# Optimization experiments

Hardware: AMD Instinct MI355X
Metric: run time of the kernel (lower is better)

The kernel has to match this reference:

```python
import jax, jax.numpy as jnp
import numpy as np

SIGMA = 1
KSIZE = SIGMA * 4 + 1  # 5
EPS = 1e-5

def _gauss_kernel1d(ksize, sigma):
    half = (ksize - 1) * 0.5
    x = jnp.linspace(-half, half, ksize)
    pdf = jnp.exp(-0.5 * (x / sigma) ** 2)
    return pdf / pdf.sum()

def _blur_axis(x, kernel, axis):
    # 'same' zero-padded 1D correlation along `axis` (grouped conv equivalent)
    pad = (kernel.shape[0] - 1) // 2
    cfg = [(0, 0)] * x.ndim
    cfg[axis] = (pad, pad)
    xp = jnp.pad(x, cfg)
    n = x.shape[axis]
    out = jnp.zeros_like(x)
    for i in range(kernel.shape[0]):
        out = out + kernel[i] * jax.lax.slice_in_dim(xp, i, i + n, axis=axis)
    return out

def gaussian_blur3d(x):  # x: [B,C,D,H,W]
    k = _gauss_kernel1d(KSIZE, SIGMA).astype(x.dtype)
    for ax in (2, 3, 4):
        x = _blur_axis(x, k, ax)
    return x

def lncc(I, J):
    bI, bJ = gaussian_blur3d(I), gaussian_blur3d(J)
    cross = gaussian_blur3d(I * J) - bI * bJ
    varI = jax.nn.relu(gaussian_blur3d(I * I) - bI ** 2) + EPS
    varJ = jax.nn.relu(gaussian_blur3d(J * J) - bJ ** 2) + EPS
    return jnp.mean(1.0 - cross / jnp.sqrt(varI * varJ))

def warp(img, phi):
    # trilinear grid_sample, zeros padding, align_corners=True
    # img: [B,C,D,H,W]; phi: [B,3,D,H,W] normalized coords (z,y,x) in [-1,1]
    B, C, D, H, W = img.shape
    scale = jnp.array([D - 1, H - 1, W - 1], img.dtype).reshape(1, 3, 1, 1, 1)
    coords = (phi + 1.0) * 0.5 * scale
    z, y, x = coords[:, 0], coords[:, 1], coords[:, 2]
    z0 = jnp.floor(z).astype(jnp.int32)
    y0 = jnp.floor(y).astype(jnp.int32)
    x0 = jnp.floor(x).astype(jnp.int32)
    fz, fy, fx = z - z0, y - y0, x - x0
    gather = jax.vmap(lambda im, zz, yy, xx: im[:, zz, yy, xx])
    out = jnp.zeros((B, C, D, H, W), img.dtype)
    for dz in (0, 1):
        for dy in (0, 1):
            for dx in (0, 1):
                zi, yi, xi = z0 + dz, y0 + dy, x0 + dx
                w = (fz if dz else 1 - fz) * (fy if dy else 1 - fy) * (fx if dx else 1 - fx)
                valid = ((zi >= 0) & (zi < D) & (yi >= 0) & (yi < H) & (xi >= 0) & (xi < W)).astype(img.dtype)
                zc = jnp.clip(zi, 0, D - 1)
                yc = jnp.clip(yi, 0, H - 1)
                xc = jnp.clip(xi, 0, W - 1)
                out = out + gather(img, zc, yc, xc) * (w * valid)[:, None]
    return out

def dice_loss(a, b):
    B = a.shape[0]
    af = a.reshape(B, -1)
    bf = b.reshape(B, -1)
    inter = jnp.sum(af * bf, axis=1)
    dice = (2.0 * inter + EPS) / (jnp.sum(af, axis=1) + jnp.sum(bf, axis=1) + EPS)
    return jnp.mean(1.0 - dice)

def identity_grid(size, batch, dtype):
    axes = [jnp.linspace(-1.0, 1.0, s, dtype=dtype) for s in size]
    grid = jnp.stack(jnp.meshgrid(*axes, indexing='ij'), axis=0)  # [3,D,H,W]
    return jnp.broadcast_to(grid[None], (batch,) + grid.shape)

def mse(a, b):
    return jnp.mean((a - b) ** 2)

def setup_inputs() -> dict:
    key = jax.random.key(0)
    ks = jax.random.split(key, 7)
    D = 128
    sp = (1, 3, D, D, D)
    si = (1, 1, D, D, D)
    return {
        'phi_AB': jax.random.normal(ks[0], sp, jnp.float32),
        'phi_BA': jax.random.normal(ks[1], sp, jnp.float32),
        'image_A': jax.random.normal(ks[2], si, jnp.float32),
        'image_B': jax.random.normal(ks[3], si, jnp.float32),
        'label_A': jax.random.uniform(ks[4], si, jnp.float32),
        'label_B': jax.random.uniform(ks[5], si, jnp.float32),
        'noise': jax.random.normal(ks[6], sp, jnp.float32),
    }

def reference(phi_AB, phi_BA, image_A, image_B, label_A, label_B, noise):
    lam = 128.0
    B = phi_AB.shape[0]
    size = phi_AB.shape[2:]
    idg = identity_grid(size, B, phi_AB.dtype)
    Ieps = idg + noise * (1.0 / size[-1])
    fwd = warp(warp(Ieps, phi_AB), phi_BA)
    bwd = warp(warp(Ieps, phi_BA), phi_AB)
    ic_loss = mse(Ieps, fwd) + mse(Ieps, bwd)
    warped_A = warp(image_A, phi_AB)
    warped_B = warp(image_B, phi_BA)
    sim_loss = lncc(warped_A, image_B) + lncc(image_A, warped_B)
    wlA = warp(label_A, phi_AB)
    wlB = warp(label_B, phi_BA)
    d_loss = dice_loss(wlA, label_B) + dice_loss(label_A, wlB)
    return lam * ic_loss + sim_loss + d_loss
```

## Files before the change

kernel.cpp:

```cpp
#include <hip/hip_runtime.h>


#define DSZ 128
#define DD  (DSZ*DSZ)
#define NVOX (DSZ*DSZ*DSZ)
#define NBLK (NVOX/256)
#define EPSF 1e-5f

#define KW0 0.054488684549642945f
#define KW1 0.24420134200323337f
#define KW2 0.40261994689424736f
#define KW3 0.24420134200323337f
#define KW4 0.054488684549642945f

#define PSTRIDE 8192

__device__ __forceinline__ double warp_red(double v) {
#pragma unroll
  for (int o = 32; o > 0; o >>= 1) v += __shfl_down(v, o, 64);
  return v;
}

__device__ __forceinline__ void block_part1(double a, double* p) {
  __shared__ double s[4];
  const int lane = threadIdx.x & 63, wid = threadIdx.x >> 6;
  a = warp_red(a);
  if (lane == 0) s[wid] = a;
  __syncthreads();
  if (threadIdx.x == 0) p[blockIdx.x] = s[0] + s[1] + s[2] + s[3];
}

__device__ __forceinline__ void block_part3(double a, double b, double c,
                                            double* p0, double* p1, double* p2) {
  __shared__ double s[3][4];
  const int lane = threadIdx.x & 63, wid = threadIdx.x >> 6;
  a = warp_red(a); b = warp_red(b); c = warp_red(c);
  if (lane == 0) { s[0][wid] = a; s[1][wid] = b; s[2][wid] = c; }
  __syncthreads();
  if (threadIdx.x == 0) {
    p0[blockIdx.x] = s[0][0] + s[0][1] + s[0][2] + s[0][3];
    p1[blockIdx.x] = s[1][0] + s[1][1] + s[1][2] + s[1][3];
    p2[blockIdx.x] = s[2][0] + s[2][1] + s[2][2] + s[2][3];
  }
}

__global__ void __launch_bounds__(256) k_pack(
    const float* __restrict__ noise, const float* __restrict__ imgA,
    const float* __restrict__ labA, const float* __restrict__ imgB,
    const float* __restrict__ labB, float4* __restrict__ S) {
  const int v = blockIdx.x * 256 + threadIdx.x;
  float4 a, b;
  a.x = noise[v]; a.y = noise[NVOX + v]; a.z = noise[2*NVOX + v]; a.w = imgA[v];
  b.x = labA[v];  b.y = imgB[v];         b.z = labB[v];           b.w = 0.0f;
  S[2*v] = a; S[2*v + 1] = b;
}

struct AxisPrep {
  int c0, c1;
  float w0, w1;
};
__device__ __forceinline__ AxisPrep axis_prep(float p) {
  AxisPrep r;
  const float pf = floorf(p);
  const int i0 = (int)pf;
  const float f = p - pf;
  const bool v0 = (i0 >= 0) && (i0 < DSZ);
  const bool v1 = (i0 + 1 >= 0) && (i0 + 1 < DSZ);
  r.c0 = min(max(i0, 0), DSZ - 1);
  r.c1 = min(max(i0 + 1, 0), DSZ - 1);
  r.w0 = v0 ? (1.0f - f) : 0.0f;
  r.w1 = v1 ? f : 0.0f;
  return r;
}

__global__ void __launch_bounds__(256) k_warp_first(
    const float* __restrict__ phiAB, const float* __restrict__ phiBA,
    const float4* __restrict__ S,
    const float* __restrict__ labA, const float* __restrict__ labB,
    float4* __restrict__ W1, float4* __restrict__ W2,
    float* __restrict__ wA, float* __restrict__ wB,
    double* __restrict__ P) {
  const int dir = blockIdx.y;
  const float* __restrict__ phi  = dir ? phiBA : phiAB;
  const float* __restrict__ olbl = dir ? labA  : labB;
  float4* __restrict__ W    = dir ? W2 : W1;
  float*  __restrict__ wimg = dir ? wB : wA;
  double* __restrict__ p    = P + (size_t)(dir ? 3 : 0) * PSTRIDE;

  const int v = blockIdx.x * 256 + threadIdx.x;
  const float ob = olbl[v];
  const float z = (phi[v]          + 1.0f) * 0.5f * 127.0f;
  const float y = (phi[NVOX + v]   + 1.0f) * 0.5f * 127.0f;
  const float x = (phi[2*NVOX + v] + 1.0f) * 0.5f * 127.0f;
  const int z0 = (int)floorf(z), y0 = (int)floorf(y), x0 = (int)floorf(x);
  float o0 = 0.f, o1 = 0.f, o2 = 0.f, oi = 0.f, ol = 0.f;
  if (z0 >= -1 && z0 < DSZ && y0 >= -1 && y0 < DSZ && x0 >= -1 && x0 < DSZ) {
    const AxisPrep az = axis_prep(z), ay = axis_prep(y), ax = axis_prep(x);
    const int zc[2] = {az.c0, az.c1}; const float wz[2] = {az.w0, az.w1};
    const int yc[2] = {ay.c0, ay.c1}; const float wy[2] = {ay.w0, ay.w1};
    const int xc[2] = {ax.c0, ax.c1}; const float wx[2] = {ax.w0, ax.w1};

    float4 g0[8], g1[8];
#pragma unroll
    for (int k = 0; k < 8; k++) {
      const int idx = zc[k >> 2] * DD + yc[(k >> 1) & 1] * DSZ + xc[k & 1];
      g0[k] = S[2 * idx];
      g1[k] = S[2 * idx + 1];
    }
#pragma unroll
    for (int k = 0; k < 8; k++) {
      const int iz = zc[k >> 2], iy = yc[(k >> 1) & 1], ix = xc[k & 1];
      const float w = wz[k >> 2] * wy[(k >> 1) & 1] * wx[k & 1];
      const float e0 = (-1.0f + iz * (2.0f/127.0f)) + g0[k].x * (1.0f/128.0f);
      const float e1 = (-1.0f + iy * (2.0f/127.0f)) + g0[k].y * (1.0f/128.0f);
      const float e2 = (-1.0f + ix * (2.0f/127.0f)) + g0[k].z * (1.0f/128.0f);
      o0 += e0 * w; o1 += e1 * w; o2 += e2 * w;
      const float iv = dir ? g1[k].y : g0[k].w;
      const float lv = dir ? g1[k].z : g1[k].x;
      oi += iv * w;
      ol += lv * w;
    }
  }
  W[v] = make_float4(o0, o1, o2, 0.0f);
  wimg[v] = oi;
  block_part3((double)(ol * ob), (double)ol, (double)ob,
              p, p + PSTRIDE, p + 2 * PSTRIDE);
}

__global__ void __launch_bounds__(256) k_warp_second_mse(
    const float* __restrict__ phiAB, const float* __restrict__ phiBA,
    const float4* __restrict__ W1, const float4* __restrict__ W2,
    const float* __restrict__ noise, double* __restrict__ P) {
  const int dir = blockIdx.y;
  const float* __restrict__ phi   = dir ? phiAB : phiBA;
  const float4* __restrict__ Wsrc = dir ? W2 : W1;
  double* __restrict__ p = P + (size_t)(6 + dir) * PSTRIDE;

  const int v = blockIdx.x * 256 + threadIdx.x;
  const float z = (phi[v]          + 1.0f) * 0.5f * 127.0f;
  const float y = (phi[NVOX + v]   + 1.0f) * 0.5f * 127.0f;
  const float x = (phi[2*NVOX + v] + 1.0f) * 0.5f * 127.0f;
  const int z0 = (int)floorf(z), y0 = (int)floorf(y), x0 = (int)floorf(x);
  float f0 = 0.f, f1 = 0.f, f2 = 0.f;
  if (z0 >= -1 && z0 < DSZ && y0 >= -1 && y0 < DSZ && x0 >= -1 && x0 < DSZ) {
    const AxisPrep az = axis_prep(z), ay = axis_prep(y), ax = axis_prep(x);
    const int zc[2] = {az.c0, az.c1}; const float wz[2] = {az.w0, az.w1};
    const int yc[2] = {ay.c0, ay.c1}; const float wy[2] = {ay.w0, ay.w1};
    const int xc[2] = {ax.c0, ax.c1}; const float wx[2] = {ax.w0, ax.w1};

    float4 g[8];
#pragma unroll
    for (int k = 0; k < 8; k++) {
      const int idx = zc[k >> 2] * DD + yc[(k >> 1) & 1] * DSZ + xc[k & 1];
      g[k] = Wsrc[idx];
    }
#pragma unroll
    for (int k = 0; k < 8; k++) {
      const float w = wz[k >> 2] * wy[(k >> 1) & 1] * wx[k & 1];
      f0 += g[k].x * w; f1 += g[k].y * w; f2 += g[k].z * w;
    }
  }
  const int zi = v >> 14, yi = (v >> 7) & 127, xi = v & 127;
  const float e0 = (-1.0f + zi * (2.0f/127.0f)) + noise[v]          * (1.0f/128.0f);
  const float e1 = (-1.0f + yi * (2.0f/127.0f)) + noise[NVOX + v]   * (1.0f/128.0f);
  const float e2 = (-1.0f + xi * (2.0f/127.0f)) + noise[2*NVOX + v] * (1.0f/128.0f);
  const float d0 = e0 - f0, d1 = e1 - f1, d2 = e2 - f2;
  block_part1((double)(d0*d0) + (double)(d1*d1) + (double)(d2*d2), p);
}

__global__ void __launch_bounds__(256) k_lncc(
    const float* __restrict__ wA, const float* __restrict__ imgB,
    const float* __restrict__ imgA, const float* __restrict__ wB,
    double* __restrict__ P) {
  const int pair = blockIdx.y;
  const float* __restrict__ I = pair ? imgA : wA;
  const float* __restrict__ J = pair ? wB : imgB;
  double* __restrict__ p = P + (size_t)(8 + pair) * PSTRIDE;

  const int bx = blockIdx.x;
  const int zi = bx & 127;
  const int y0 = (bx >> 7) * 8;

  __shared__ float zb[5][12][128];
  __shared__ float yb[5][8][128];
  const int t = threadIdx.x;
  const float K[5] = {KW0, KW1, KW2, KW3, KW4};

  for (int pp = t; pp < 12 * 128; pp += 256) {
    const int r = pp >> 7, x = pp & 127;
    const int y = y0 + r - 2;
    float a0 = 0.f, a1 = 0.f, a2 = 0.f, a3 = 0.f, a4 = 0.f;
    if (y >= 0 && y < DSZ) {
      const int base = y * DSZ + x;
#pragma unroll
      for (int s = 0; s < 5; s++) {
        const int zz = zi + s - 2;
        if (zz >= 0 && zz < DSZ) {
          const float iv = I[zz * DD + base], jv = J[zz * DD + base];
          const float k = K[s];
          a0 += k * iv; a1 += k * jv; a2 += k * (iv * jv);
          a3 += k * (iv * iv); a4 += k * (jv * jv);
        }
      }
    }
    zb[0][r][x] = a0; zb[1][r][x] = a1; zb[2][r][x] = a2;
    zb[3][r][x] = a3; zb[4][r][x] = a4;
  }
  __syncthreads();

  for (int pp = t; pp < 8 * 128; pp += 256) {
    const int r = pp >> 7, x = pp & 127;
#pragma unroll
    for (int c = 0; c < 5; c++) {
      yb[c][r][x] = KW0 * zb[c][r][x] + KW1 * zb[c][r + 1][x] + KW2 * zb[c][r + 2][x]
                  + KW3 * zb[c][r + 3][x] + KW4 * zb[c][r + 4][x];
    }
  }
  __syncthreads();

  double lsum = 0.0;
  for (int pp = t; pp < 8 * 128; pp += 256) {
    const int r = pp >> 7, x = pp & 127;
    float b[5];
#pragma unroll
    for (int c = 0; c < 5; c++) {
      float s = 0.f;
#pragma unroll
      for (int u = 0; u < 5; u++) {
        const int xx = x + u - 2;
        if (xx >= 0 && xx < DSZ) s += K[u] * yb[c][r][xx];
      }
      b[c] = s;
    }
    const float cross = b[2] - b[0] * b[1];
    const float varI = fmaxf(b[3] - b[0] * b[0], 0.0f) + EPSF;
    const float varJ = fmaxf(b[4] - b[1] * b[1], 0.0f) + EPSF;
    lsum += (double)(1.0f - cross / sqrtf(varI * varJ));
  }
  block_part1(lsum, p);
}

__global__ void __launch_bounds__(256) k_reduce(
    const double* __restrict__ P, double* __restrict__ acc) {
  const int c = blockIdx.x;
  const int n = (c >= 8) ? 2048 : 8192;
  const double* src = P + (size_t)c * PSTRIDE;
  double s = 0.0;
  for (int i = threadIdx.x; i < n; i += 256) s += src[i];
  __shared__ double sh[4];
  const int lane = threadIdx.x & 63, wid = threadIdx.x >> 6;
  s = warp_red(s);
  if (lane == 0) sh[wid] = s;
  __syncthreads();
  if (threadIdx.x == 0) acc[c] = sh[0] + sh[1] + sh[2] + sh[3];
}

__global__ void k_final(const double* __restrict__ acc, float* __restrict__ out) {
  const double n1 = (double)NVOX;
  const double n3 = 3.0 * n1;
  const double ic  = acc[6] / n3 + acc[7] / n3;
  const double sim = acc[8] / n1 + acc[9] / n1;
  const double dA = (2.0 * acc[0] + 1e-5) / (acc[1] + acc[2] + 1e-5);
  const double dB = (2.0 * acc[3] + 1e-5) / (acc[4] + acc[5] + 1e-5);
  out[0] = (float)(128.0 * ic + sim + (1.0 - dA) + (1.0 - dB));
}

extern "C" void kernel_launch(void* const* d_in, const int* in_sizes, int n_in,
                              void* d_out, int out_size, void* d_ws, size_t ws_size,
                              hipStream_t stream) {
  (void)in_sizes; (void)n_in; (void)out_size; (void)ws_size;
  const float* phiAB = (const float*)d_in[0];
  const float* phiBA = (const float*)d_in[1];
  const float* imgA  = (const float*)d_in[2];
  const float* imgB  = (const float*)d_in[3];
  const float* labA  = (const float*)d_in[4];
  const float* labB  = (const float*)d_in[5];
  const float* noise = (const float*)d_in[6];
  float* out = (float*)d_out;

  char* ws = (char*)d_ws;
  double* acc = (double*)ws;
  double* P   = acc + 16;
  float4* S  = (float4*)(ws + (1 << 20));
  float4* W1 = S + 2 * (size_t)NVOX;
  float4* W2 = W1 + (size_t)NVOX;
  float*  wA = (float*)(W2 + (size_t)NVOX);
  float*  wB = wA + NVOX;

  k_pack<<<NBLK, 256, 0, stream>>>(noise, imgA, labA, imgB, labB, S);

  k_warp_first<<<dim3(NBLK, 2), 256, 0, stream>>>(
      phiAB, phiBA, S, labA, labB, W1, W2, wA, wB, P);

  k_warp_second_mse<<<dim3(NBLK, 2), 256, 0, stream>>>(
      phiAB, phiBA, W1, W2, noise, P);

  k_lncc<<<dim3(2048, 2), 256, 0, stream>>>(wA, imgB, imgA, wB, P);

  k_reduce<<<10, 256, 0, stream>>>(P, acc);

  k_final<<<1, 1, 0, stream>>>(acc, out);
}
```

Before: 487.3 us.

## Fuse second warp/MSE and LNCC into one interleaved kernel launch

Merges the second-warp MSE kernel and the LNCC blur kernel into one launch. Blocks are interleaved two warp blocks to one LNCC block, so the gather-bound and compute/LDS-bound work can share the GPU at the same time. The LNCC tile is halved from 8 to 4 rows per block, which doubles its block count and raises the z/y halo overhead. Shared-memory allocation is now the union of both paths, which may reduce occupancy for the warp blocks.

```diff
diff --git a/kernel.cpp b/kernel.cpp
--- a/kernel.cpp
+++ b/kernel.cpp
@@ -21,26 +21,27 @@
   return v;
 }
 
-__device__ __forceinline__ void block_part1(double a, double* p) {
-  __shared__ double s[4];
+__device__ __forceinline__ void block_part1(double a, double* p, int slot) {
+  __shared__ double s1[4];
   const int lane = threadIdx.x & 63, wid = threadIdx.x >> 6;
   a = warp_red(a);
-  if (lane == 0) s[wid] = a;
+  if (lane == 0) s1[wid] = a;
   __syncthreads();
-  if (threadIdx.x == 0) p[blockIdx.x] = s[0] + s[1] + s[2] + s[3];
+  if (threadIdx.x == 0) p[slot] = s1[0] + s1[1] + s1[2] + s1[3];
 }
 
 __device__ __forceinline__ void block_part3(double a, double b, double c,
-                                            double* p0, double* p1, double* p2) {
-  __shared__ double s[3][4];
+                                            double* p0, double* p1, double* p2,
+                                            int slot) {
+  __shared__ double s3[3][4];
   const int lane = threadIdx.x & 63, wid = threadIdx.x >> 6;
   a = warp_red(a); b = warp_red(b); c = warp_red(c);
-  if (lane == 0) { s[0][wid] = a; s[1][wid] = b; s[2][wid] = c; }
+  if (lane == 0) { s3[0][wid] = a; s3[1][wid] = b; s3[2][wid] = c; }
   __syncthreads();
   if (threadIdx.x == 0) {
-    p0[blockIdx.x] = s[0][0] + s[0][1] + s[0][2] + s[0][3];
-    p1[blockIdx.x] = s[1][0] + s[1][1] + s[1][2] + s[1][3];
-    p2[blockIdx.x] = s[2][0] + s[2][1] + s[2][2] + s[2][3];
+    p0[slot] = s3[0][0] + s3[0][1] + s3[0][2] + s3[0][3];
+    p1[slot] = s3[1][0] + s3[1][1] + s3[1][2] + s3[1][3];
+    p2[slot] = s3[2][0] + s3[2][1] + s3[2][2] + s3[2][3];
   }
 }
 
@@ -124,126 +125,131 @@
   W[v] = make_float4(o0, o1, o2, 0.0f);
   wimg[v] = oi;
   block_part3((double)(ol * ob), (double)ol, (double)ob,
-              p, p + PSTRIDE, p + 2 * PSTRIDE);
-}
-
-__global__ void __launch_bounds__(256) k_warp_second_mse(
+              p, p + PSTRIDE, p + 2 * PSTRIDE, blockIdx.x);
+}
+
+__global__ void __launch_bounds__(256) k_phase2(
     const float* __restrict__ phiAB, const float* __restrict__ phiBA,
     const float4* __restrict__ W1, const float4* __restrict__ W2,
-    const float* __restrict__ noise, double* __restrict__ P) {
-  const int dir = blockIdx.y;
-  const float* __restrict__ phi   = dir ? phiAB : phiBA;
-  const float4* __restrict__ Wsrc = dir ? W2 : W1;
-  double* __restrict__ p = P + (size_t)(6 + dir) * PSTRIDE;
-
-  const int v = blockIdx.x * 256 + threadIdx.x;
-  const float z = (phi[v]          + 1.0f) * 0.5f * 127.0f;
-  const float y = (phi[NVOX + v]   + 1.0f) * 0.5f * 127.0f;
-  const float x = (phi[2*NVOX + v] + 1.0f) * 0.5f * 127.0f;
-  const int z0 = (int)floorf(z), y0 = (int)floorf(y), x0 = (int)floorf(x);
-  float f0 = 0.f, f1 = 0.f, f2 = 0.f;
-  if (z0 >= -1 && z0 < DSZ && y0 >= -1 && y0 < DSZ && x0 >= -1 && x0 < DSZ) {
-    const AxisPrep az = axis_prep(z), ay = axis_prep(y), ax = axis_prep(x);
-    const int zc[2] = {az.c0, az.c1}; const float wz[2] = {az.w0, az.w1};
-    const int yc[2] = {ay.c0, ay.c1}; const float wy[2] = {ay.w0, ay.w1};
-    const int xc[2] = {ax.c0, ax.c1}; const float wx[2] = {ax.w0, ax.w1};
-
-    float4 g[8];
-#pragma unroll
-    for (int k = 0; k < 8; k++) {
-      const int idx = zc[k >> 2] * DD + yc[(k >> 1) & 1] * DSZ + xc[k & 1];
-      g[k] = Wsrc[idx];
-    }
-#pragma unroll
-    for (int k = 0; k < 8; k++) {
-      const float w = wz[k >> 2] * wy[(k >> 1) & 1] * wx[k & 1];
-      f0 += g[k].x * w; f1 += g[k].y * w; f2 += g[k].z * w;
-    }
-  }
-  const int zi = v >> 14, yi = (v >> 7) & 127, xi = v & 127;
-  const float e0 = (-1.0f + zi * (2.0f/127.0f)) + noise[v]          * (1.0f/128.0f);
-  const float e1 = (-1.0f + yi * (2.0f/127.0f)) + noise[NVOX + v]   * (1.0f/128.0f);
-  const float e2 = (-1.0f + xi * (2.0f/127.0f)) + noise[2*NVOX + v] * (1.0f/128.0f);
-  const float d0 = e0 - f0, d1 = e1 - f1, d2 = e2 - f2;
-  block_part1((double)(d0*d0) + (double)(d1*d1) + (double)(d2*d2), p);
-}
-
-__global__ void __launch_bounds__(256) k_lncc(
+    const float* __restrict__ noise,
     const float* __restrict__ wA, const float* __restrict__ imgB,
     const float* __restrict__ imgA, const float* __restrict__ wB,
     double* __restrict__ P) {
-  const int pair = blockIdx.y;
-  const float* __restrict__ I = pair ? imgA : wA;
-  const float* __restrict__ J = pair ? wB : imgB;
-  double* __restrict__ p = P + (size_t)(8 + pair) * PSTRIDE;
-
-  const int bx = blockIdx.x;
-  const int zi = bx & 127;
-  const int y0 = (bx >> 7) * 8;
-
-  __shared__ float zb[5][12][128];
-  __shared__ float yb[5][8][128];
-  const int t = threadIdx.x;
-  const float K[5] = {KW0, KW1, KW2, KW3, KW4};
-
-  for (int pp = t; pp < 12 * 128; pp += 256) {
-    const int r = pp >> 7, x = pp & 127;
-    const int y = y0 + r - 2;
-    float a0 = 0.f, a1 = 0.f, a2 = 0.f, a3 = 0.f, a4 = 0.f;
-    if (y >= 0 && y < DSZ) {
-      const int base = y * DSZ + x;
-#pragma unroll
-      for (int s = 0; s < 5; s++) {
-        const int zz = zi + s - 2;
-        if (zz >= 0 && zz < DSZ) {
-          const float iv = I[zz * DD + base], jv = J[zz * DD + base];
-          const float k = K[s];
-          a0 += k * iv; a1 += k * jv; a2 += k * (iv * jv);
-          a3 += k * (iv * iv); a4 += k * (jv * jv);
+  __shared__ float zb[5][8][128];
+  __shared__ float yb[5][4][128];
+  const int bid = blockIdx.x;
+  const int grp = bid / 3, rem = bid - grp * 3;
+
+  if (rem < 2) {
+    const int gid = grp * 2 + rem;
+    const int dir = gid >> 13;
+    const int vb  = gid & 8191;
+    const float* __restrict__ phi   = dir ? phiAB : phiBA;
+    const float4* __restrict__ Wsrc = dir ? W2 : W1;
+    double* __restrict__ p = P + (size_t)(6 + dir) * PSTRIDE;
+
+    const int v = vb * 256 + threadIdx.x;
+    const float z = (phi[v]          + 1.0f) * 0.5f * 127.0f;
+    const float y = (phi[NVOX + v]   + 1.0f) * 0.5f * 127.0f;
+    const float x = (phi[2*NVOX + v] + 1.0f) * 0.5f * 127.0f;
+    const int z0 = (int)floorf(z), y0 = (int)floorf(y), x0 = (int)floorf(x);
+    float f0 = 0.f, f1 = 0.f, f2 = 0.f;
+    if (z0 >= -1 && z0 < DSZ && y0 >= -1 && y0 < DSZ && x0 >= -1 && x0 < DSZ) {
+      const AxisPrep az = axis_prep(z), ay = axis_prep(y), ax = axis_prep(x);
+      const int zc[2] = {az.c0, az.c1}; const float wz[2] = {az.w0, az.w1};
+      const int yc[2] = {ay.c0, ay.c1}; const float wy[2] = {ay.w0, ay.w1};
+      const int xc[2] = {ax.c0, ax.c1}; const float wx[2] = {ax.w0, ax.w1};
+
+      float4 g[8];
+#pragma unroll
+      for (int k = 0; k < 8; k++) {
+        const int idx = zc[k >> 2] * DD + yc[(k >> 1) & 1] * DSZ + xc[k & 1];
+        g[k] = Wsrc[idx];
+      }
+#pragma unroll
+      for (int k = 0; k < 8; k++) {
+        const float w = wz[k >> 2] * wy[(k >> 1) & 1] * wx[k & 1];
+        f0 += g[k].x * w; f1 += g[k].y * w; f2 += g[k].z * w;
+      }
+    }
+    const int zi = v >> 14, yi = (v >> 7) & 127, xi = v & 127;
+    const float e0 = (-1.0f + zi * (2.0f/127.0f)) + noise[v]          * (1.0f/128.0f);
+    const float e1 = (-1.0f + yi * (2.0f/127.0f)) + noise[NVOX + v]   * (1.0f/128.0f);
+    const float e2 = (-1.0f + xi * (2.0f/127.0f)) + noise[2*NVOX + v] * (1.0f/128.0f);
+    const float d0 = e0 - f0, d1 = e1 - f1, d2 = e2 - f2;
+    block_part1((double)(d0*d0) + (double)(d1*d1) + (double)(d2*d2), p, vb);
+  } else {
+    const int lid = grp;
+    const int pair = lid >> 12;
+    const int bx   = lid & 4095;
+    const float* __restrict__ I = pair ? imgA : wA;
+    const float* __restrict__ J = pair ? wB : imgB;
+    double* __restrict__ p = P + (size_t)(8 + pair) * PSTRIDE;
+
+    const int zi = bx & 127;
+    const int y0 = (bx >> 7) * 4;
+    const int t = threadIdx.x;
+    const float K[5] = {KW0, KW1, KW2, KW3, KW4};
+
+    for (int pp = t; pp < 8 * 128; pp += 256) {
+      const int r = pp >> 7, x = pp & 127;
+      const int y = y0 + r - 2;
+      float a0 = 0.f, a1 = 0.f, a2 = 0.f, a3 = 0.f, a4 = 0.f;
+      if (y >= 0 && y < DSZ) {
+        const int base = y * DSZ + x;
+#pragma unroll
+        for (int s = 0; s < 5; s++) {
+          const int zz = zi + s - 2;
+          if (zz >= 0 && zz < DSZ) {
+            const float iv = I[zz * DD + base], jv = J[zz * DD + base];
+            const float k = K[s];
+            a0 += k * iv; a1 += k * jv; a2 += k * (iv * jv);
+            a3 += k * (iv * iv); a4 += k * (jv * jv);
+          }
         }
       }
-    }
-    zb[0][r][x] = a0; zb[1][r][x] = a1; zb[2][r][x] = a2;
-    zb[3][r][x] = a3; zb[4][r][x] = a4;
+      zb[0][r][x] = a0; zb[1][r][x] = a1; zb[2][r][x] = a2;
+      zb[3][r][x] = a3; zb[4][r][x] = a4;
+    }
+    __syncthreads();
+
+    for (int pp = t; pp < 4 * 128; pp += 256) {
+      const int r = pp >> 7, x = pp & 127;
+#pragma unroll
+      for (int c = 0; c < 5; c++) {
+        yb[c][r][x] = KW0 * zb[c][r][x] + KW1 * zb[c][r + 1][x] + KW2 * zb[c][r + 2][x]
+                    + KW3 * zb[c][r + 3][x] + KW4 * zb[c][r + 4][x];
+      }
+    }
+    __syncthreads();
+
+    double lsum = 0.0;
+    for (int pp = t; pp < 4 * 128; pp += 256) {
+      const int r = pp >> 7, x = pp & 127;
+      float b[5];
+#pragma unroll
+      for (int c = 0; c < 5; c++) {
+        float s = 0.f;
+#pragma unroll
+        for (int u = 0; u < 5; u++) {
+          const int xx = x + u - 2;
+          if (xx >= 0 && xx < DSZ) s += K[u] * yb[c][r][xx];
+        }
+        b[c] = s;
+      }
+      const float cross = b[2] - b[0] * b[1];
+      const float varI = fmaxf(b[3] - b[0] * b[0], 0.0f) + EPSF;
+      const float varJ = fmaxf(b[4] - b[1] * b[1], 0.0f) + EPSF;
+      lsum += (double)(1.0f - cross / sqrtf(varI * varJ));
+    }
+    block_part1(lsum, p, bx);
   }
-  __syncthreads();
-
-  for (int pp = t; pp < 8 * 128; pp += 256) {
-    const int r = pp >> 7, x = pp & 127;
-#pragma unroll
-    for (int c = 0; c < 5; c++) {
-      yb[c][r][x] = KW0 * zb[c][r][x] + KW1 * zb[c][r + 1][x] + KW2 * zb[c][r + 2][x]
-                  + KW3 * zb[c][r + 3][x] + KW4 * zb[c][r + 4][x];
-    }
-  }
-  __syncthreads();
-
-  double lsum = 0.0;
-  for (int pp = t; pp < 8 * 128; pp += 256) {
-    const int r = pp >> 7, x = pp & 127;
-    float b[5];
-#pragma unroll
-    for (int c = 0; c < 5; c++) {
-      float s = 0.f;
-#pragma unroll
-      for (int u = 0; u < 5; u++) {
-        const int xx = x + u - 2;
-        if (xx >= 0 && xx < DSZ) s += K[u] * yb[c][r][xx];
-      }
-      b[c] = s;
-    }
-    const float cross = b[2] - b[0] * b[1];
-    const float varI = fmaxf(b[3] - b[0] * b[0], 0.0f) + EPSF;
-    const float varJ = fmaxf(b[4] - b[1] * b[1], 0.0f) + EPSF;
-    lsum += (double)(1.0f - cross / sqrtf(varI * varJ));
-  }
-  block_part1(lsum, p);
 }
 
 __global__ void __launch_bounds__(256) k_reduce(
     const double* __restrict__ P, double* __restrict__ acc) {
   const int c = blockIdx.x;
-  const int n = (c >= 8) ? 2048 : 8192;
+  const int n = (c >= 8) ? 4096 : 8192;
   const double* src = P + (size_t)c * PSTRIDE;
   double s = 0.0;
   for (int i = threadIdx.x; i < n; i += 256) s += src[i];
@@ -292,10 +298,8 @@
   k_warp_first<<<dim3(NBLK, 2), 256, 0, stream>>>(
       phiAB, phiBA, S, labA, labB, W1, W2, wA, wB, P);
 
-  k_warp_second_mse<<<dim3(NBLK, 2), 256, 0, stream>>>(
-      phiAB, phiBA, W1, W2, noise, P);
-
-  k_lncc<<<dim3(2048, 2), 256, 0, stream>>>(wA, imgB, imgA, wB, P);
+  k_phase2<<<24576, 256, 0, stream>>>(
+      phiAB, phiBA, W1, W2, noise, wA, imgB, imgA, wB, P);
 
   k_reduce<<<10, 256, 0, stream>>>(P, acc);
 
```

Result: faster. 419.3 us (-14.0%).
